# Performance work log

Hardware: AMD Instinct MI355X
Metric: run time of the kernel (lower is better)

The kernel has to match this reference:

```python
import jax, jax.numpy as jnp
import numpy as np

NUM_EXPERTS = 64
TOP_K = 8
HIDDEN = 2048
MLP = 768
TOKENS = 1024


def setup_inputs() -> dict:
    key = jax.random.key(0)
    ks = jax.random.split(key, 5)
    hidden_states = jax.random.normal(ks[0], (TOKENS, HIDDEN), dtype=jnp.float32)
    # lecun-normal-ish scaling (std = 1/sqrt(fan_in))
    router_w = jax.random.normal(ks[1], (HIDDEN, NUM_EXPERTS), dtype=jnp.float32) / np.sqrt(HIDDEN)
    gate_proj = jax.random.normal(ks[2], (NUM_EXPERTS, HIDDEN, MLP), dtype=jnp.float32) / np.sqrt(HIDDEN)
    up_proj = jax.random.normal(ks[3], (NUM_EXPERTS, HIDDEN, MLP), dtype=jnp.float32) / np.sqrt(HIDDEN)
    down_proj = jax.random.normal(ks[4], (NUM_EXPERTS, MLP, HIDDEN), dtype=jnp.float32) / np.sqrt(MLP)
    return {
        "hidden_states": hidden_states,
        "router_w": router_w,
        "gate_proj": gate_proj,
        "up_proj": up_proj,
        "down_proj": down_proj,
    }


def reference(hidden_states, router_w, gate_proj, up_proj, down_proj):
    # Router: [T, E]
    router_logits = hidden_states @ router_w
    # Top-k routing, softmax renormalized over the selected k (norm_topk_prob=True)
    routing_weights, selected_experts = jax.lax.top_k(router_logits, k=TOP_K)
    routing_weights = jax.nn.softmax(routing_weights, axis=-1)  # [T, k]

    sel_flat = selected_experts.ravel()  # [T*k] int32
    # Duplicate each token for each of its k experts: [T*k, H]
    x_exp = jnp.repeat(hidden_states, TOP_K, axis=0)

    # prepare_routing: sort token copies by expert id, count per-expert group sizes
    sort_idx = jnp.argsort(sel_flat)          # stable sort of expert ids
    x_sorted = x_exp[sort_idx]                # [T*k, H] grouped by expert
    group_sizes = jnp.zeros((NUM_EXPERTS,), dtype=jnp.int32).at[sel_flat].add(1)
    unsort_idx = jnp.argsort(sort_idx)

    # Grouped GEMMs (megablox-style) via ragged_dot
    gate_out = jax.lax.ragged_dot(x_sorted, gate_proj, group_sizes)   # [T*k, M]
    up_out = jax.lax.ragged_dot(x_sorted, up_proj, group_sizes)       # [T*k, M]
    down_out = jax.lax.ragged_dot(jax.nn.silu(gate_out) * up_out, down_proj, group_sizes)  # [T*k, H]

    # Unsort back to (token, k) order and combine with routing weights
    unsorted = down_out[unsort_idx].reshape(-1, TOP_K, HIDDEN)
    return jnp.sum(unsorted * routing_weights[..., None], axis=1)  # [T, H]
```

## Files before the change

kernel.cpp:

```cpp
#include <hip/hip_runtime.h>
#include <hip/hip_bf16.h>

#define T_TOKENS 1024
#define HID      2048
#define NEXP     64
#define TOPK     8
#define MLP      768
#define NPAIR    (T_TOKENS * TOPK)

typedef __bf16 bf16x8 __attribute__((ext_vector_type(8)));
typedef float  f32x4  __attribute__((ext_vector_type(4)));
typedef unsigned int u32x2 __attribute__((ext_vector_type(2)));
typedef unsigned int u32x4 __attribute__((ext_vector_type(4)));

#define LDK 40

static __device__ __forceinline__ unsigned short f2bf(float f) {
    __hip_bfloat16 h = __float2bfloat16(f);
    unsigned short u;
    __builtin_memcpy(&u, &h, sizeof(u));
    return u;
}
static __device__ __forceinline__ unsigned int pk2bf(float a, float b) {
    return (unsigned int)f2bf(a) | ((unsigned int)f2bf(b) << 16);
}

__global__ __launch_bounds__(256) void cvt_hs_kernel(
    const float* __restrict__ hs, unsigned short* __restrict__ xb)
{
    int i = (blockIdx.x * 256 + threadIdx.x) * 8;
    f32x4 a = *(const f32x4*)(hs + i);
    f32x4 b = *(const f32x4*)(hs + i + 4);
    u32x4 v;
    v[0] = pk2bf(a[0], a[1]); v[1] = pk2bf(a[2], a[3]);
    v[2] = pk2bf(b[0], b[1]); v[3] = pk2bf(b[2], b[3]);
    *(u32x4*)(xb + i) = v;
}

__global__ __launch_bounds__(256) void router_topk_kernel(
    const float* __restrict__ hs, const float* __restrict__ rw,
    int* __restrict__ sel, float* __restrict__ wts)
{
    const int lane = threadIdx.x & 63;
    const int tg   = threadIdx.x >> 6;
    const int t    = blockIdx.x * 4 + tg;

    const float4* x4 = (const float4*)(hs + (size_t)t * HID);
    float acc = 0.f;
    for (int h4 = 0; h4 < HID / 4; ++h4) {
        float4 xv = x4[h4];
        int hb = h4 * 4 * NEXP + lane;
        acc += xv.x * rw[hb] + xv.y * rw[hb + NEXP]
             + xv.z * rw[hb + 2 * NEXP] + xv.w * rw[hb + 3 * NEXP];
    }

    float v = acc;
    float tv[TOPK]; int ti[TOPK];
    for (int i = 0; i < TOPK; ++i) {
        float m = v; int mi = lane;
        for (int off = 32; off > 0; off >>= 1) {
            float om  = __shfl_xor(m, off, 64);
            int   omi = __shfl_xor(mi, off, 64);
            if (om > m || (om == m && omi < mi)) { m = om; mi = omi; }
        }
        tv[i] = m; ti[i] = mi;
        if (lane == mi) v = -__builtin_inff();
    }
    if (lane == 0) {
        float mx = tv[0], s = 0.f, e[TOPK];
        for (int i = 0; i < TOPK; ++i) { e[i] = __expf(tv[i] - mx); s += e[i]; }
        float inv = 1.f / s;
        for (int i = 0; i < TOPK; ++i) {
            wts[t * TOPK + i] = e[i] * inv;
            sel[t * TOPK + i] = ti[i];
        }
    }
}

__global__ void count_kernel(const int* __restrict__ sel, int* __restrict__ counts)
{
    int p = blockIdx.x * 256 + threadIdx.x;
    if (p < NPAIR) atomicAdd(&counts[sel[p]], 1);
}

__global__ void scan_kernel(const int* __restrict__ counts,
                            int* __restrict__ offsets, int* __restrict__ cursor)
{
    if (threadIdx.x == 0) {
        int s = 0;
        for (int e = 0; e < NEXP; ++e) { offsets[e] = s; cursor[e] = s; s += counts[e]; }
        offsets[NEXP] = s;
    }
}

__global__ void scatter_kernel(const int* __restrict__ sel,
                               int* __restrict__ cursor, int* __restrict__ rows)
{
    int p = blockIdx.x * 256 + threadIdx.x;
    if (p < NPAIR) {
        int e = sel[p];
        int pos = atomicAdd(&cursor[e], 1);
        rows[pos] = p;
    }
}

__global__ __launch_bounds__(512) void gateup_kernel(
    const unsigned short* __restrict__ xb, const float* __restrict__ gw,
    const float* __restrict__ uw, const int* __restrict__ offsets,
    const int* __restrict__ rows, unsigned short* __restrict__ hb)
{
    const int bid = blockIdx.x;
    const int sw  = (bid & 7) * 96 + (bid >> 3);
    const int e   = sw / 12;
    const int n0  = (sw % 12) * 64;

    const int r0 = offsets[e];
    const int nrows = offsets[e + 1] - r0;
    if (nrows <= 0) return;

    __shared__ __align__(16) float smemf[12800];
    unsigned short* smem = (unsigned short*)smemf;

    const int thr  = threadIdx.x;
    const int wave = thr >> 6;
    const int lane = thr & 63;
    const int wg   = wave & 3;
    const int isUp = wave >> 2;
    const int fr   = lane & 15;
    const int fq   = lane >> 4;

    const int ar = thr >> 3;
    const int ac = (thr & 7) * 4;

    const int wk2 = thr & 15;
    const int wnq = (thr & 255) >> 4;
    const float* wsrc = (thr >= 256 ? uw : gw)
        + (size_t)e * HID * MLP + (size_t)(2 * wk2) * MLP + n0 + wnq * 4;
    const int mofs = (thr >= 256) ? 10240 : 7680;

    const int NS = HID / 32;

    for (int m0 = 0; m0 < nrows; m0 += 192) {
        const unsigned short *ap0, *ap1, *ap2;
        bool av0, av1, av2;
        {
            int gr0 = m0 + ar, gr1 = m0 + ar + 64, gr2 = m0 + ar + 128;
            av0 = gr0 < nrows; av1 = gr1 < nrows; av2 = gr2 < nrows;
            int p0 = av0 ? rows[r0 + gr0] : 0;
            int p1 = av1 ? rows[r0 + gr1] : 0;
            int p2 = av2 ? rows[r0 + gr2] : 0;
            ap0 = xb + (size_t)(p0 >> 3) * HID + ac;
            ap1 = xb + (size_t)(p1 >> 3) * HID + ac;
            ap2 = xb + (size_t)(p2 >> 3) * HID + ac;
        }

        u32x2 va0, va1, va2;
        f32x4 w0e, w1e, w0o, w1o;
        const u32x2 z2 = (u32x2){0u, 0u};
        const f32x4 fz = (f32x4){0.f, 0.f, 0.f, 0.f};

        auto LOAD_A = [&](int s) {
            va0 = av0 ? *(const u32x2*)(ap0 + s * 32) : z2;
            va1 = av1 ? *(const u32x2*)(ap1 + s * 32) : z2;
            va2 = av2 ? *(const u32x2*)(ap2 + s * 32) : z2;
        };
        auto WRITE_A = [&](int s) {
            unsigned short* b = smem + (s & 1) * 12800;
            *(u32x2*)(b + ar * LDK + ac) = va0;
            *(u32x2*)(b + (ar + 64) * LDK + ac) = va1;
            *(u32x2*)(b + (ar + 128) * LDK + ac) = va2;
        };
        auto LOAD_WE = [&](int s) {
            const float* wp = wsrc + (size_t)s * 32 * MLP;
            w0e = *(const f32x4*)wp;  w1e = *(const f32x4*)(wp + MLP);
        };
        auto LOAD_WO = [&](int s) {
            const float* wp = wsrc + (size_t)s * 32 * MLP;
            w0o = *(const f32x4*)wp;  w1o = *(const f32x4*)(wp + MLP);
        };
        auto WRITE_WE = [&](int s) {
            unsigned short* wb = smem + (s & 1) * 12800 + mofs;
            #pragma unroll
            for (int i = 0; i < 4; ++i)
                *(unsigned int*)(wb + (wnq * 4 + i) * LDK + 2 * wk2) = pk2bf(w0e[i], w1e[i]);
        };
        auto WRITE_WO = [&](int s) {
            unsigned short* wb = smem + (s & 1) * 12800 + mofs;
            #pragma unroll
            for (int i = 0; i < 4; ++i)
                *(unsigned int*)(wb + (wnq * 4 + i) * LDK + 2 * wk2) = pk2bf(w0o[i], w1o[i]);
        };

        f32x4 acc[3][4];
        #pragma unroll
        for (int ms = 0; ms < 3; ++ms)
            #pragma unroll
            for (int ns = 0; ns < 4; ++ns) acc[ms][ns] = fz;

        const int rem = nrows - m0 - wg * 48;

        auto DOSTEP = [&](const unsigned short* bb) {
            const unsigned short* wbb = bb + mofs;
            bf16x8 aF0, aF1, aF2, wF[4];
            #pragma unroll
            for (int ns = 0; ns < 4; ++ns)
                wF[ns] = *(const bf16x8*)(wbb + (ns * 16 + fr) * LDK + fq * 8);
            aF0 = *(const bf16x8*)(bb + (wg * 48 + fr) * LDK + fq * 8);
            aF1 = *(const bf16x8*)(bb + (wg * 48 + 16 + fr) * LDK + fq * 8);
            aF2 = *(const bf16x8*)(bb + (wg * 48 + 32 + fr) * LDK + fq * 8);
            return (void)0, (void)aF0, (void)aF1, (void)aF2, (void)wF;
        };
        (void)DOSTEP;

        LOAD_WE(0);
        LOAD_WO(1);
        LOAD_A(0);
        WRITE_WE(0);
        WRITE_A(0);
        LOAD_A(1);
        asm volatile("s_waitcnt lgkmcnt(0)" ::: "memory");
        __builtin_amdgcn_s_barrier();

        #define GU_MFMA(BB)                                                          \
        {                                                                            \
            const unsigned short* wbb = (BB) + mofs;                                 \
            bf16x8 aF0, aF1, aF2, wF0, wF1, wF2, wF3;                                \
            wF0 = *(const bf16x8*)(wbb + (0 * 16 + fr) * LDK + fq * 8);              \
            wF1 = *(const bf16x8*)(wbb + (1 * 16 + fr) * LDK + fq * 8);              \
            wF2 = *(const bf16x8*)(wbb + (2 * 16 + fr) * LDK + fq * 8);              \
            wF3 = *(const bf16x8*)(wbb + (3 * 16 + fr) * LDK + fq * 8);              \
            aF0 = *(const bf16x8*)((BB) + (wg * 48 + fr) * LDK + fq * 8);            \
            aF1 = *(const bf16x8*)((BB) + (wg * 48 + 16 + fr) * LDK + fq * 8);       \
            aF2 = *(const bf16x8*)((BB) + (wg * 48 + 32 + fr) * LDK + fq * 8);       \
            MFMA_BLOCK(aF0, aF1, aF2, wF0, wF1, wF2, wF3)                            \
        }
        #define MFMA_BLOCK(A0, A1, A2, W0, W1, W2, W3)                               \
            if (rem > 0) {                                                           \
                acc[0][0] = __builtin_amdgcn_mfma_f32_16x16x32_bf16(A0, W0, acc[0][0], 0, 0, 0); \
                acc[0][1] = __builtin_amdgcn_mfma_f32_16x16x32_bf16(A0, W1, acc[0][1], 0, 0, 0); \
                acc[0][2] = __builtin_amdgcn_mfma_f32_16x16x32_bf16(A0, W2, acc[0][2], 0, 0, 0); \
                acc[0][3] = __builtin_amdgcn_mfma_f32_16x16x32_bf16(A0, W3, acc[0][3], 0, 0, 0); \
            }                                                                        \
            if (rem > 16) {                                                          \
                acc[1][0] = __builtin_amdgcn_mfma_f32_16x16x32_bf16(A1, W0, acc[1][0], 0, 0, 0); \
                acc[1][1] = __builtin_amdgcn_mfma_f32_16x16x32_bf16(A1, W1, acc[1][1], 0, 0, 0); \
                acc[1][2] = __builtin_amdgcn_mfma_f32_16x16x32_bf16(A1, W2, acc[1][2], 0, 0, 0); \
                acc[1][3] = __builtin_amdgcn_mfma_f32_16x16x32_bf16(A1, W3, acc[1][3], 0, 0, 0); \
            }                                                                        \
            if (rem > 32) {                                                          \
                acc[2][0] = __builtin_amdgcn_mfma_f32_16x16x32_bf16(A2, W0, acc[2][0], 0, 0, 0); \
                acc[2][1] = __builtin_amdgcn_mfma_f32_16x16x32_bf16(A2, W1, acc[2][1], 0, 0, 0); \
                acc[2][2] = __builtin_amdgcn_mfma_f32_16x16x32_bf16(A2, W2, acc[2][2], 0, 0, 0); \
                acc[2][3] = __builtin_amdgcn_mfma_f32_16x16x32_bf16(A2, W3, acc[2][3], 0, 0, 0); \
            }

        for (int s = 0; s < NS; s += 2) {
            {
                if (s + 2 < NS) LOAD_WE(s + 2);
                GU_MFMA(smem)
                WRITE_WO(s + 1);
                WRITE_A(s + 1);
                if (s + 2 < NS) LOAD_A(s + 2);
                asm volatile("s_waitcnt lgkmcnt(0)" ::: "memory");
                __builtin_amdgcn_s_barrier();
            }
            {
                if (s + 3 < NS) LOAD_WO(s + 3);
                GU_MFMA(smem + 12800)
                if (s + 2 < NS) { WRITE_WE(s + 2); WRITE_A(s + 2); }
                if (s + 3 < NS) LOAD_A(s + 3);
                asm volatile("s_waitcnt lgkmcnt(0)" ::: "memory");
                __builtin_amdgcn_s_barrier();
            }
        }
        #undef GU_MFMA
        #undef MFMA_BLOCK

        float* xbf = smemf;
        if (isUp) {
            #pragma unroll
            for (int ms = 0; ms < 3; ++ms)
                #pragma unroll
                for (int i = 0; i < 4; ++i) {
                    int lrow = wg * 48 + ms * 16 + fq * 4 + i;
                    #pragma unroll
                    for (int ns = 0; ns < 4; ++ns)
                        xbf[lrow * 65 + ns * 16 + fr] = acc[ms][ns][i];
                }
        }
        __syncthreads();
        if (!isUp) {
            #pragma unroll
            for (int ms = 0; ms < 3; ++ms)
                #pragma unroll
                for (int i = 0; i < 4; ++i) {
                    int lrow = wg * 48 + ms * 16 + fq * 4 + i;
                    int grow = m0 + lrow;
                    if (grow < nrows) {
                        unsigned short* drow = hb + (size_t)(r0 + grow) * MLP + n0;
                        #pragma unroll
                        for (int ns = 0; ns < 4; ++ns) {
                            float g = acc[ms][ns][i];
                            float u = xbf[lrow * 65 + ns * 16 + fr];
                            float h = g * u / (1.f + __expf(-g));
                            drow[ns * 16 + fr] = f2bf(h);
                        }
                    }
                }
        }
        __syncthreads();
    }
}

__global__ __launch_bounds__(256) void down_kernel(
    const unsigned short* __restrict__ hb, const float* __restrict__ dw,
    const int* __restrict__ offsets, const int* __restrict__ rows,
    const float* __restrict__ wts, float* __restrict__ out)
{
    const int bid = blockIdx.x;
    const int sw  = (bid & 7) * 256 + (bid >> 3);
    const int e   = sw >> 5;
    const int n0  = (sw & 31) * 64;

    const int r0 = offsets[e];
    const int nrows = offsets[e + 1] - r0;
    if (nrows <= 0) return;

    __shared__ __align__(16) float smemf[10240];
    unsigned short* smem = (unsigned short*)smemf;

    const int thr  = threadIdx.x;
    const int wave = thr >> 6;
    const int lane = thr & 63;
    const int fr   = lane & 15;
    const int fq   = lane >> 4;

    const int ar = thr >> 2;
    const int ac = (thr & 3) * 8;

    const int wk2 = thr & 15;
    const int wnq = thr >> 4;
    const float* wsrc = dw + (size_t)e * MLP * HID + (size_t)(2 * wk2) * HID + n0 + wnq * 4;

    const int NS = MLP / 32;

    for (int m0 = 0; m0 < nrows; m0 += 192) {
        const bool av0 = (m0 + ar)       < nrows;
        const bool av1 = (m0 + ar + 64)  < nrows;
        const bool av2 = (m0 + ar + 128) < nrows;
        const unsigned short* hp0 = hb + (size_t)(r0 + m0 + ar) * MLP + ac;
        const unsigned short* hp1 = hp0 + (size_t)64  * MLP;
        const unsigned short* hp2 = hp0 + (size_t)128 * MLP;

        u32x4 ua0, ua1, ua2;
        f32x4 w0e, w1e, w0o, w1o;
        const u32x4 uz = (u32x4){0u, 0u, 0u, 0u};
        const f32x4 fz = (f32x4){0.f, 0.f, 0.f, 0.f};

        auto LOAD_A = [&](int s) {
            ua0 = av0 ? *(const u32x4*)(hp0 + s * 32) : uz;
            ua1 = av1 ? *(const u32x4*)(hp1 + s * 32) : uz;
            ua2 = av2 ? *(const u32x4*)(hp2 + s * 32) : uz;
        };
        auto WRITE_A = [&](int s) {
            unsigned short* b = smem + (s & 1) * 10240;
            *(u32x4*)(b + ar * LDK + ac) = ua0;
            *(u32x4*)(b + (ar + 64) * LDK + ac) = ua1;
            *(u32x4*)(b + (ar + 128) * LDK + ac) = ua2;
        };
        auto LOAD_WE = [&](int s) {
            const float* wp = wsrc + (size_t)s * 32 * HID;
            w0e = *(const f32x4*)wp;  w1e = *(const f32x4*)(wp + HID);
        };
        auto LOAD_WO = [&](int s) {
            const float* wp = wsrc + (size_t)s * 32 * HID;
            w0o = *(const f32x4*)wp;  w1o = *(const f32x4*)(wp + HID);
        };
        auto WRITE_WE = [&](int s) {
            unsigned short* wb = smem + (s & 1) * 10240 + 7680;
            #pragma unroll
            for (int i = 0; i < 4; ++i)
                *(unsigned int*)(wb + (wnq * 4 + i) * LDK + 2 * wk2) = pk2bf(w0e[i], w1e[i]);
        };
        auto WRITE_WO = [&](int s) {
            unsigned short* wb = smem + (s & 1) * 10240 + 7680;
            #pragma unroll
            for (int i = 0; i < 4; ++i)
                *(unsigned int*)(wb + (wnq * 4 + i) * LDK + 2 * wk2) = pk2bf(w0o[i], w1o[i]);
        };

        f32x4 acc[3][4];
        #pragma unroll
        for (int ms = 0; ms < 3; ++ms)
            #pragma unroll
            for (int ns = 0; ns < 4; ++ns) acc[ms][ns] = fz;

        const int rem = nrows - m0 - wave * 48;

        LOAD_WE(0);
        LOAD_WO(1);
        LOAD_A(0);
        WRITE_WE(0);
        WRITE_A(0);
        LOAD_A(1);
        asm volatile("s_waitcnt lgkmcnt(0)" ::: "memory");
        __builtin_amdgcn_s_barrier();

        #define DN_MFMA(BB)                                                          \
        {                                                                            \
            const unsigned short* wbb = (BB) + 7680;                                 \
            bf16x8 aF0, aF1, aF2, wF0, wF1, wF2, wF3;                                \
            wF0 = *(const bf16x8*)(wbb + (0 * 16 + fr) * LDK + fq * 8);              \
            wF1 = *(const bf16x8*)(wbb + (1 * 16 + fr) * LDK + fq * 8);              \
            wF2 = *(const bf16x8*)(wbb + (2 * 16 + fr) * LDK + fq * 8);              \
            wF3 = *(const bf16x8*)(wbb + (3 * 16 + fr) * LDK + fq * 8);              \
            aF0 = *(const bf16x8*)((BB) + (wave * 48 + fr) * LDK + fq * 8);          \
            aF1 = *(const bf16x8*)((BB) + (wave * 48 + 16 + fr) * LDK + fq * 8);     \
            aF2 = *(const bf16x8*)((BB) + (wave * 48 + 32 + fr) * LDK + fq * 8);     \
            if (rem > 0) {                                                           \
                acc[0][0] = __builtin_amdgcn_mfma_f32_16x16x32_bf16(aF0, wF0, acc[0][0], 0, 0, 0); \
                acc[0][1] = __builtin_amdgcn_mfma_f32_16x16x32_bf16(aF0, wF1, acc[0][1], 0, 0, 0); \
                acc[0][2] = __builtin_amdgcn_mfma_f32_16x16x32_bf16(aF0, wF2, acc[0][2], 0, 0, 0); \
                acc[0][3] = __builtin_amdgcn_mfma_f32_16x16x32_bf16(aF0, wF3, acc[0][3], 0, 0, 0); \
            }                                                                        \
            if (rem > 16) {                                                          \
                acc[1][0] = __builtin_amdgcn_mfma_f32_16x16x32_bf16(aF1, wF0, acc[1][0], 0, 0, 0); \
                acc[1][1] = __builtin_amdgcn_mfma_f32_16x16x32_bf16(aF1, wF1, acc[1][1], 0, 0, 0); \
                acc[1][2] = __builtin_amdgcn_mfma_f32_16x16x32_bf16(aF1, wF2, acc[1][2], 0, 0, 0); \
                acc[1][3] = __builtin_amdgcn_mfma_f32_16x16x32_bf16(aF1, wF3, acc[1][3], 0, 0, 0); \
            }                                                                        \
            if (rem > 32) {                                                          \
                acc[2][0] = __builtin_amdgcn_mfma_f32_16x16x32_bf16(aF2, wF0, acc[2][0], 0, 0, 0); \
                acc[2][1] = __builtin_amdgcn_mfma_f32_16x16x32_bf16(aF2, wF1, acc[2][1], 0, 0, 0); \
                acc[2][2] = __builtin_amdgcn_mfma_f32_16x16x32_bf16(aF2, wF2, acc[2][2], 0, 0, 0); \
                acc[2][3] = __builtin_amdgcn_mfma_f32_16x16x32_bf16(aF2, wF3, acc[2][3], 0, 0, 0); \
            }                                                                        \
        }

        for (int s = 0; s < NS; s += 2) {
            {
                if (s + 2 < NS) LOAD_WE(s + 2);
                DN_MFMA(smem)
                WRITE_WO(s + 1);
                WRITE_A(s + 1);
                if (s + 2 < NS) LOAD_A(s + 2);
                asm volatile("s_waitcnt lgkmcnt(0)" ::: "memory");
                __builtin_amdgcn_s_barrier();
            }
            {
                if (s + 3 < NS) LOAD_WO(s + 3);
                DN_MFMA(smem + 10240)
                if (s + 2 < NS) { WRITE_WE(s + 2); WRITE_A(s + 2); }
                if (s + 3 < NS) LOAD_A(s + 3);
                asm volatile("s_waitcnt lgkmcnt(0)" ::: "memory");
                __builtin_amdgcn_s_barrier();
            }
        }
        #undef DN_MFMA

        #pragma unroll
        for (int ms = 0; ms < 3; ++ms) {
            #pragma unroll
            for (int i = 0; i < 4; ++i) {
                int lrow = wave * 48 + ms * 16 + fq * 4 + i;
                int grow = m0 + lrow;
                if (grow < nrows) {
                    int p  = rows[r0 + grow];
                    float w = wts[p];
                    float* orow = out + (size_t)(p >> 3) * HID + n0;
                    #pragma unroll
                    for (int ns = 0; ns < 4; ++ns)
                        atomicAdd(orow + ns * 16 + fr, acc[ms][ns][i] * w);
                }
            }
        }
    }
}

extern "C" void kernel_launch(void* const* d_in, const int* in_sizes, int n_in,
                              void* d_out, int out_size, void* d_ws, size_t ws_size,
                              hipStream_t stream)
{
    const float* hs = (const float*)d_in[0];
    const float* rw = (const float*)d_in[1];
    const float* gw = (const float*)d_in[2];
    const float* uw = (const float*)d_in[3];
    const float* dw = (const float*)d_in[4];
    float* out = (float*)d_out;

    char* ws = (char*)d_ws;
    int*   sel     = (int*)(ws);
    float* wts     = (float*)(ws + 32768);
    int*   counts  = (int*)(ws + 65536);
    int*   offsets = (int*)(ws + 65792);
    int*   cursor  = (int*)(ws + 66304);
    int*   rows    = (int*)(ws + 66560);
    unsigned short* xb = (unsigned short*)(ws + 99328);
    unsigned short* hb = (unsigned short*)(ws + 99328 + 4194304);

    hipMemsetAsync(out, 0, (size_t)T_TOKENS * HID * sizeof(float), stream);
    hipMemsetAsync(counts, 0, NEXP * sizeof(int), stream);

    cvt_hs_kernel<<<T_TOKENS * HID / (256 * 8), 256, 0, stream>>>(hs, xb);
    router_topk_kernel<<<T_TOKENS / 4, 256, 0, stream>>>(hs, rw, sel, wts);
    count_kernel<<<NPAIR / 256, 256, 0, stream>>>(sel, counts);
    scan_kernel<<<1, 64, 0, stream>>>(counts, offsets, cursor);
    scatter_kernel<<<NPAIR / 256, 256, 0, stream>>>(sel, cursor, rows);
    gateup_kernel<<<768, 512, 0, stream>>>(xb, gw, uw, offsets, rows, hb);
    down_kernel<<<2048, 256, 0, stream>>>(hb, dw, offsets, rows, wts, out);
}
```

Baseline: 1.237 ms.

## Fuse routing prep kernels, widen per-wave tiles and halve GEMM block counts

Folds the fp32-to-bf16 conversion of hidden states into the router kernel, and merges the count, scan and scatter steps into one single-block kernel that uses shared-memory atomics. The gate/up kernel moves from 512 to 256 threads, with each wave covering 96 rows instead of 48. The down kernel now covers a 128-wide N tile with 2x2 wave tiling, which halves the grid. Weight loads are widened to 8 floats per thread. The aim is to cut launch overhead and raise MFMA work per LDS fragment load, at the cost of more accumulator registers and possible occupancy loss.

```diff
diff --git a/kernel.cpp b/kernel.cpp
--- a/kernel.cpp
+++ b/kernel.cpp
@@ -25,25 +25,28 @@
     return (unsigned int)f2bf(a) | ((unsigned int)f2bf(b) << 16);
 }
 
-__global__ __launch_bounds__(256) void cvt_hs_kernel(
-    const float* __restrict__ hs, unsigned short* __restrict__ xb)
-{
-    int i = (blockIdx.x * 256 + threadIdx.x) * 8;
-    f32x4 a = *(const f32x4*)(hs + i);
-    f32x4 b = *(const f32x4*)(hs + i + 4);
-    u32x4 v;
-    v[0] = pk2bf(a[0], a[1]); v[1] = pk2bf(a[2], a[3]);
-    v[2] = pk2bf(b[0], b[1]); v[3] = pk2bf(b[2], b[3]);
-    *(u32x4*)(xb + i) = v;
-}
-
 __global__ __launch_bounds__(256) void router_topk_kernel(
     const float* __restrict__ hs, const float* __restrict__ rw,
-    int* __restrict__ sel, float* __restrict__ wts)
+    int* __restrict__ sel, float* __restrict__ wts, unsigned short* __restrict__ xb)
 {
     const int lane = threadIdx.x & 63;
     const int tg   = threadIdx.x >> 6;
     const int t    = blockIdx.x * 4 + tg;
+
+    {
+        const float* xr = hs + (size_t)t * HID;
+        unsigned short* xw = xb + (size_t)t * HID;
+        #pragma unroll
+        for (int c = 0; c < 4; ++c) {
+            int i = (lane + c * 64) * 8;
+            f32x4 a = *(const f32x4*)(xr + i);
+            f32x4 b = *(const f32x4*)(xr + i + 4);
+            u32x4 v;
+            v[0] = pk2bf(a[0], a[1]); v[1] = pk2bf(a[2], a[3]);
+            v[2] = pk2bf(b[0], b[1]); v[3] = pk2bf(b[2], b[3]);
+            *(u32x4*)(xw + i) = v;
+        }
+    }
 
     const float4* x4 = (const float4*)(hs + (size_t)t * HID);
     float acc = 0.f;
@@ -77,34 +80,36 @@
     }
 }
 
-__global__ void count_kernel(const int* __restrict__ sel, int* __restrict__ counts)
+__global__ __launch_bounds__(1024) void route_kernel(
+    const int* __restrict__ sel, int* __restrict__ offsets, int* __restrict__ rows)
 {
-    int p = blockIdx.x * 256 + threadIdx.x;
-    if (p < NPAIR) atomicAdd(&counts[sel[p]], 1);
-}
-
-__global__ void scan_kernel(const int* __restrict__ counts,
-                            int* __restrict__ offsets, int* __restrict__ cursor)
-{
-    if (threadIdx.x == 0) {
+    __shared__ int cnt[NEXP];
+    __shared__ int cur[NEXP];
+    const int t = threadIdx.x;
+    if (t < NEXP) cnt[t] = 0;
+    __syncthreads();
+    int e[8];
+    const int p0 = t * 8;
+    #pragma unroll
+    for (int j = 0; j < 8; ++j) {
+        e[j] = sel[p0 + j];
+        atomicAdd(&cnt[e[j]], 1);
+    }
+    __syncthreads();
+    if (t == 0) {
         int s = 0;
-        for (int e = 0; e < NEXP; ++e) { offsets[e] = s; cursor[e] = s; s += counts[e]; }
+        for (int i = 0; i < NEXP; ++i) { cur[i] = s; offsets[i] = s; s += cnt[i]; }
         offsets[NEXP] = s;
     }
-}
-
-__global__ void scatter_kernel(const int* __restrict__ sel,
-                               int* __restrict__ cursor, int* __restrict__ rows)
-{
-    int p = blockIdx.x * 256 + threadIdx.x;
-    if (p < NPAIR) {
-        int e = sel[p];
-        int pos = atomicAdd(&cursor[e], 1);
-        rows[pos] = p;
-    }
-}
-
-__global__ __launch_bounds__(512) void gateup_kernel(
+    __syncthreads();
+    #pragma unroll
+    for (int j = 0; j < 8; ++j) {
+        int pos = atomicAdd(&cur[e[j]], 1);
+        rows[pos] = p0 + j;
+    }
+}
+
+__global__ __launch_bounds__(256, 2) void gateup_kernel(
     const unsigned short* __restrict__ xb, const float* __restrict__ gw,
     const float* __restrict__ uw, const int* __restrict__ offsets,
     const int* __restrict__ rows, unsigned short* __restrict__ hb)
@@ -124,19 +129,21 @@
     const int thr  = threadIdx.x;
     const int wave = thr >> 6;
     const int lane = thr & 63;
-    const int wg   = wave & 3;
-    const int isUp = wave >> 2;
+    const int wg   = wave & 1;
+    const int isUp = wave >> 1;
     const int fr   = lane & 15;
     const int fq   = lane >> 4;
-
-    const int ar = thr >> 3;
-    const int ac = (thr & 7) * 4;
-
-    const int wk2 = thr & 15;
-    const int wnq = (thr & 255) >> 4;
-    const float* wsrc = (thr >= 256 ? uw : gw)
-        + (size_t)e * HID * MLP + (size_t)(2 * wk2) * MLP + n0 + wnq * 4;
-    const int mofs = (thr >= 256) ? 10240 : 7680;
+    const int mofs_c = isUp ? 10240 : 7680;
+
+    const int ar = thr >> 2;
+    const int ac = (thr & 3) * 8;
+
+    const int tt   = thr & 127;
+    const int wk2  = tt & 15;
+    const int nst  = (tt >> 4) * 8;
+    const float* wsrc = (thr >= 128 ? uw : gw)
+        + (size_t)e * HID * MLP + (size_t)(2 * wk2) * MLP + n0 + nst;
+    const int mofs_s = (thr >= 128) ? 10240 : 7680;
 
     const int NS = HID / 32;
 
@@ -154,63 +161,77 @@
             ap2 = xb + (size_t)(p2 >> 3) * HID + ac;
         }
 
-        u32x2 va0, va1, va2;
-        f32x4 w0e, w1e, w0o, w1o;
-        const u32x2 z2 = (u32x2){0u, 0u};
+        u32x4 va0, va1, va2;
+        f32x4 wAe, wBe, wCe, wDe, wAo, wBo, wCo, wDo;
+        const u32x4 uz = (u32x4){0u, 0u, 0u, 0u};
         const f32x4 fz = (f32x4){0.f, 0.f, 0.f, 0.f};
 
         auto LOAD_A = [&](int s) {
-            va0 = av0 ? *(const u32x2*)(ap0 + s * 32) : z2;
-            va1 = av1 ? *(const u32x2*)(ap1 + s * 32) : z2;
-            va2 = av2 ? *(const u32x2*)(ap2 + s * 32) : z2;
+            va0 = av0 ? *(const u32x4*)(ap0 + s * 32) : uz;
+            va1 = av1 ? *(const u32x4*)(ap1 + s * 32) : uz;
+            va2 = av2 ? *(const u32x4*)(ap2 + s * 32) : uz;
         };
         auto WRITE_A = [&](int s) {
             unsigned short* b = smem + (s & 1) * 12800;
-            *(u32x2*)(b + ar * LDK + ac) = va0;
-            *(u32x2*)(b + (ar + 64) * LDK + ac) = va1;
-            *(u32x2*)(b + (ar + 128) * LDK + ac) = va2;
+            *(u32x4*)(b + ar * LDK + ac) = va0;
+            *(u32x4*)(b + (ar + 64) * LDK + ac) = va1;
+            *(u32x4*)(b + (ar + 128) * LDK + ac) = va2;
         };
         auto LOAD_WE = [&](int s) {
             const float* wp = wsrc + (size_t)s * 32 * MLP;
-            w0e = *(const f32x4*)wp;  w1e = *(const f32x4*)(wp + MLP);
+            wAe = *(const f32x4*)wp;        wBe = *(const f32x4*)(wp + 4);
+            wCe = *(const f32x4*)(wp + MLP); wDe = *(const f32x4*)(wp + MLP + 4);
         };
         auto LOAD_WO = [&](int s) {
             const float* wp = wsrc + (size_t)s * 32 * MLP;
-            w0o = *(const f32x4*)wp;  w1o = *(const f32x4*)(wp + MLP);
+            wAo = *(const f32x4*)wp;        wBo = *(const f32x4*)(wp + 4);
+            wCo = *(const f32x4*)(wp + MLP); wDo = *(const f32x4*)(wp + MLP + 4);
         };
         auto WRITE_WE = [&](int s) {
-            unsigned short* wb = smem + (s & 1) * 12800 + mofs;
-            #pragma unroll
-            for (int i = 0; i < 4; ++i)
-                *(unsigned int*)(wb + (wnq * 4 + i) * LDK + 2 * wk2) = pk2bf(w0e[i], w1e[i]);
+            unsigned short* wb = smem + (s & 1) * 12800 + mofs_s;
+            #pragma unroll
+            for (int j = 0; j < 4; ++j) {
+                *(unsigned int*)(wb + (nst + j) * LDK + 2 * wk2)     = pk2bf(wAe[j], wCe[j]);
+                *(unsigned int*)(wb + (nst + 4 + j) * LDK + 2 * wk2) = pk2bf(wBe[j], wDe[j]);
+            }
         };
         auto WRITE_WO = [&](int s) {
-            unsigned short* wb = smem + (s & 1) * 12800 + mofs;
-            #pragma unroll
-            for (int i = 0; i < 4; ++i)
-                *(unsigned int*)(wb + (wnq * 4 + i) * LDK + 2 * wk2) = pk2bf(w0o[i], w1o[i]);
-        };
-
-        f32x4 acc[3][4];
+            unsigned short* wb = smem + (s & 1) * 12800 + mofs_s;
+            #pragma unroll
+            for (int j = 0; j < 4; ++j) {
+                *(unsigned int*)(wb + (nst + j) * LDK + 2 * wk2)     = pk2bf(wAo[j], wCo[j]);
+                *(unsigned int*)(wb + (nst + 4 + j) * LDK + 2 * wk2) = pk2bf(wBo[j], wDo[j]);
+            }
+        };
+
+        f32x4 acc[6][4];
         #pragma unroll
-        for (int ms = 0; ms < 3; ++ms)
+        for (int ms = 0; ms < 6; ++ms)
             #pragma unroll
             for (int ns = 0; ns < 4; ++ns) acc[ms][ns] = fz;
 
-        const int rem = nrows - m0 - wg * 48;
-
-        auto DOSTEP = [&](const unsigned short* bb) {
-            const unsigned short* wbb = bb + mofs;
-            bf16x8 aF0, aF1, aF2, wF[4];
-            #pragma unroll
-            for (int ns = 0; ns < 4; ++ns)
-                wF[ns] = *(const bf16x8*)(wbb + (ns * 16 + fr) * LDK + fq * 8);
-            aF0 = *(const bf16x8*)(bb + (wg * 48 + fr) * LDK + fq * 8);
-            aF1 = *(const bf16x8*)(bb + (wg * 48 + 16 + fr) * LDK + fq * 8);
-            aF2 = *(const bf16x8*)(bb + (wg * 48 + 32 + fr) * LDK + fq * 8);
-            return (void)0, (void)aF0, (void)aF1, (void)aF2, (void)wF;
-        };
-        (void)DOSTEP;
+        const int rem = nrows - m0 - wg * 96;
+
+        auto STEP = [&](const unsigned short* bb) {
+            const unsigned short* wbb = bb + mofs_c;
+            bf16x8 wF0 = *(const bf16x8*)(wbb + (0 * 16 + fr) * LDK + fq * 8);
+            bf16x8 wF1 = *(const bf16x8*)(wbb + (1 * 16 + fr) * LDK + fq * 8);
+            bf16x8 wF2 = *(const bf16x8*)(wbb + (2 * 16 + fr) * LDK + fq * 8);
+            bf16x8 wF3 = *(const bf16x8*)(wbb + (3 * 16 + fr) * LDK + fq * 8);
+            bf16x8 aF[6];
+            #pragma unroll
+            for (int ms = 0; ms < 6; ++ms)
+                aF[ms] = *(const bf16x8*)(bb + (wg * 96 + ms * 16 + fr) * LDK + fq * 8);
+            #pragma unroll
+            for (int ms = 0; ms < 6; ++ms) {
+                if (rem > ms * 16) {
+                    acc[ms][0] = __builtin_amdgcn_mfma_f32_16x16x32_bf16(aF[ms], wF0, acc[ms][0], 0, 0, 0);
+                    acc[ms][1] = __builtin_amdgcn_mfma_f32_16x16x32_bf16(aF[ms], wF1, acc[ms][1], 0, 0, 0);
+                    acc[ms][2] = __builtin_amdgcn_mfma_f32_16x16x32_bf16(aF[ms], wF2, acc[ms][2], 0, 0, 0);
+                    acc[ms][3] = __builtin_amdgcn_mfma_f32_16x16x32_bf16(aF[ms], wF3, acc[ms][3], 0, 0, 0);
+                }
+            }
+        };
 
         LOAD_WE(0);
         LOAD_WO(1);
@@ -221,68 +242,29 @@
         asm volatile("s_waitcnt lgkmcnt(0)" ::: "memory");
         __builtin_amdgcn_s_barrier();
 
-        #define GU_MFMA(BB)                                                          \
-        {                                                                            \
-            const unsigned short* wbb = (BB) + mofs;                                 \
-            bf16x8 aF0, aF1, aF2, wF0, wF1, wF2, wF3;                                \
-            wF0 = *(const bf16x8*)(wbb + (0 * 16 + fr) * LDK + fq * 8);              \
-            wF1 = *(const bf16x8*)(wbb + (1 * 16 + fr) * LDK + fq * 8);              \
-            wF2 = *(const bf16x8*)(wbb + (2 * 16 + fr) * LDK + fq * 8);              \
-            wF3 = *(const bf16x8*)(wbb + (3 * 16 + fr) * LDK + fq * 8);              \
-            aF0 = *(const bf16x8*)((BB) + (wg * 48 + fr) * LDK + fq * 8);            \
-            aF1 = *(const bf16x8*)((BB) + (wg * 48 + 16 + fr) * LDK + fq * 8);       \
-            aF2 = *(const bf16x8*)((BB) + (wg * 48 + 32 + fr) * LDK + fq * 8);       \
-            MFMA_BLOCK(aF0, aF1, aF2, wF0, wF1, wF2, wF3)                            \
-        }
-        #define MFMA_BLOCK(A0, A1, A2, W0, W1, W2, W3)                               \
-            if (rem > 0) {                                                           \
-                acc[0][0] = __builtin_amdgcn_mfma_f32_16x16x32_bf16(A0, W0, acc[0][0], 0, 0, 0); \
-                acc[0][1] = __builtin_amdgcn_mfma_f32_16x16x32_bf16(A0, W1, acc[0][1], 0, 0, 0); \
-                acc[0][2] = __builtin_amdgcn_mfma_f32_16x16x32_bf16(A0, W2, acc[0][2], 0, 0, 0); \
-                acc[0][3] = __builtin_amdgcn_mfma_f32_16x16x32_bf16(A0, W3, acc[0][3], 0, 0, 0); \
-            }                                                                        \
-            if (rem > 16) {                                                          \
-                acc[1][0] = __builtin_amdgcn_mfma_f32_16x16x32_bf16(A1, W0, acc[1][0], 0, 0, 0); \
-                acc[1][1] = __builtin_amdgcn_mfma_f32_16x16x32_bf16(A1, W1, acc[1][1], 0, 0, 0); \
-                acc[1][2] = __builtin_amdgcn_mfma_f32_16x16x32_bf16(A1, W2, acc[1][2], 0, 0, 0); \
-                acc[1][3] = __builtin_amdgcn_mfma_f32_16x16x32_bf16(A1, W3, acc[1][3], 0, 0, 0); \
-            }                                                                        \
-            if (rem > 32) {                                                          \
-                acc[2][0] = __builtin_amdgcn_mfma_f32_16x16x32_bf16(A2, W0, acc[2][0], 0, 0, 0); \
-                acc[2][1] = __builtin_amdgcn_mfma_f32_16x16x32_bf16(A2, W1, acc[2][1], 0, 0, 0); \
-                acc[2][2] = __builtin_amdgcn_mfma_f32_16x16x32_bf16(A2, W2, acc[2][2], 0, 0, 0); \
-                acc[2][3] = __builtin_amdgcn_mfma_f32_16x16x32_bf16(A2, W3, acc[2][3], 0, 0, 0); \
-            }
-
         for (int s = 0; s < NS; s += 2) {
-            {
-                if (s + 2 < NS) LOAD_WE(s + 2);
-                GU_MFMA(smem)
-                WRITE_WO(s + 1);
-                WRITE_A(s + 1);
-                if (s + 2 < NS) LOAD_A(s + 2);
-                asm volatile("s_waitcnt lgkmcnt(0)" ::: "memory");
-                __builtin_amdgcn_s_barrier();
-            }
-            {
-                if (s + 3 < NS) LOAD_WO(s + 3);
-                GU_MFMA(smem + 12800)
-                if (s + 2 < NS) { WRITE_WE(s + 2); WRITE_A(s + 2); }
-                if (s + 3 < NS) LOAD_A(s + 3);
-                asm volatile("s_waitcnt lgkmcnt(0)" ::: "memory");
-                __builtin_amdgcn_s_barrier();
-            }
-        }
-        #undef GU_MFMA
-        #undef MFMA_BLOCK
+            if (s + 2 < NS) LOAD_WE(s + 2);
+            STEP(smem);
+            WRITE_WO(s + 1);
+            WRITE_A(s + 1);
+            if (s + 2 < NS) LOAD_A(s + 2);
+            asm volatile("s_waitcnt lgkmcnt(0)" ::: "memory");
+            __builtin_amdgcn_s_barrier();
+            if (s + 3 < NS) LOAD_WO(s + 3);
+            STEP(smem + 12800);
+            if (s + 2 < NS) { WRITE_WE(s + 2); WRITE_A(s + 2); }
+            if (s + 3 < NS) LOAD_A(s + 3);
+            asm volatile("s_waitcnt lgkmcnt(0)" ::: "memory");
+            __builtin_amdgcn_s_barrier();
+        }
 
         float* xbf = smemf;
         if (isUp) {
             #pragma unroll
-            for (int ms = 0; ms < 3; ++ms)
+            for (int ms = 0; ms < 6; ++ms)
                 #pragma unroll
                 for (int i = 0; i < 4; ++i) {
-                    int lrow = wg * 48 + ms * 16 + fq * 4 + i;
+                    int lrow = wg * 96 + ms * 16 + fq * 4 + i;
                     #pragma unroll
                     for (int ns = 0; ns < 4; ++ns)
                         xbf[lrow * 65 + ns * 16 + fr] = acc[ms][ns][i];
@@ -291,10 +273,10 @@
         __syncthreads();
         if (!isUp) {
             #pragma unroll
-            for (int ms = 0; ms < 3; ++ms)
+            for (int ms = 0; ms < 6; ++ms)
                 #pragma unroll
                 for (int i = 0; i < 4; ++i) {
-                    int lrow = wg * 48 + ms * 16 + fq * 4 + i;
+                    int lrow = wg * 96 + ms * 16 + fq * 4 + i;
                     int grow = m0 + lrow;
                     if (grow < nrows) {
                         unsigned short* drow = hb + (size_t)(r0 + grow) * MLP + n0;
@@ -312,26 +294,28 @@
     }
 }
 
-__global__ __launch_bounds__(256) void down_kernel(
+__global__ __launch_bounds__(256, 2) void down_kernel(
     const unsigned short* __restrict__ hb, const float* __restrict__ dw,
     const int* __restrict__ offsets, const int* __restrict__ rows,
     const float* __restrict__ wts, float* __restrict__ out)
 {
     const int bid = blockIdx.x;
-    const int sw  = (bid & 7) * 256 + (bid >> 3);
-    const int e   = sw >> 5;
-    const int n0  = (sw & 31) * 64;
+    const int sw  = (bid & 7) * 128 + (bid >> 3);
+    const int e   = sw >> 4;
+    const int n0  = (sw & 15) * 128;
 
     const int r0 = offsets[e];
     const int nrows = offsets[e + 1] - r0;
     if (nrows <= 0) return;
 
-    __shared__ __align__(16) float smemf[10240];
+    __shared__ __align__(16) float smemf[12800];
     unsigned short* smem = (unsigned short*)smemf;
 
     const int thr  = threadIdx.x;
     const int wave = thr >> 6;
     const int lane = thr & 63;
+    const int wg   = wave & 1;
+    const int wn   = wave >> 1;
     const int fr   = lane & 15;
     const int fq   = lane >> 4;
 
@@ -339,8 +323,8 @@
     const int ac = (thr & 3) * 8;
 
     const int wk2 = thr & 15;
-    const int wnq = thr >> 4;
-    const float* wsrc = dw + (size_t)e * MLP * HID + (size_t)(2 * wk2) * HID + n0 + wnq * 4;
+    const int nst = (thr >> 4) * 8;
+    const float* wsrc = dw + (size_t)e * MLP * HID + (size_t)(2 * wk2) * HID + n0 + nst;
 
     const int NS = MLP / 32;
 
@@ -353,7 +337,7 @@
         const unsigned short* hp2 = hp0 + (size_t)128 * MLP;
 
         u32x4 ua0, ua1, ua2;
-        f32x4 w0e, w1e, w0o, w1o;
+        f32x4 wAe, wBe, wCe, wDe, wAo, wBo, wCo, wDo;
         const u32x4 uz = (u32x4){0u, 0u, 0u, 0u};
         const f32x4 fz = (f32x4){0.f, 0.f, 0.f, 0.f};
 
@@ -363,39 +347,66 @@
             ua2 = av2 ? *(const u32x4*)(hp2 + s * 32) : uz;
         };
         auto WRITE_A = [&](int s) {
-            unsigned short* b = smem + (s & 1) * 10240;
+            unsigned short* b = smem + (s & 1) * 12800;
             *(u32x4*)(b + ar * LDK + ac) = ua0;
             *(u32x4*)(b + (ar + 64) * LDK + ac) = ua1;
             *(u32x4*)(b + (ar + 128) * LDK + ac) = ua2;
         };
         auto LOAD_WE = [&](int s) {
             const float* wp = wsrc + (size_t)s * 32 * HID;
-            w0e = *(const f32x4*)wp;  w1e = *(const f32x4*)(wp + HID);
+            wAe = *(const f32x4*)wp;        wBe = *(const f32x4*)(wp + 4);
+            wCe = *(const f32x4*)(wp + HID); wDe = *(const f32x4*)(wp + HID + 4);
         };
         auto LOAD_WO = [&](int s) {
             const float* wp = wsrc + (size_t)s * 32 * HID;
-            w0o = *(const f32x4*)wp;  w1o = *(const f32x4*)(wp + HID);
+            wAo = *(const f32x4*)wp;        wBo = *(const f32x4*)(wp + 4);
+            wCo = *(const f32x4*)(wp + HID); wDo = *(const f32x4*)(wp + HID + 4);
         };
         auto WRITE_WE = [&](int s) {
-            unsigned short* wb = smem + (s & 1) * 10240 + 7680;
-            #pragma unroll
-            for (int i = 0; i < 4; ++i)
-                *(unsigned int*)(wb + (wnq * 4 + i) * LDK + 2 * wk2) = pk2bf(w0e[i], w1e[i]);
+            unsigned short* wb = smem + (s & 1) * 12800 + 7680;
+            #pragma unroll
+            for (int j = 0; j < 4; ++j) {
+                *(unsigned int*)(wb + (nst + j) * LDK + 2 * wk2)     = pk2bf(wAe[j], wCe[j]);
+                *(unsigned int*)(wb + (nst + 4 + j) * LDK + 2 * wk2) = pk2bf(wBe[j], wDe[j]);
+            }
         };
         auto WRITE_WO = [&](int s) {
-            unsigned short* wb = smem + (s & 1) * 10240 + 7680;
-            #pragma unroll
-            for (int i = 0; i < 4; ++i)
-                *(unsigned int*)(wb + (wnq * 4 + i) * LDK + 2 * wk2) = pk2bf(w0o[i], w1o[i]);
-        };
-
-        f32x4 acc[3][4];
+            unsigned short* wb = smem + (s & 1) * 12800 + 7680;
+            #pragma unroll
+            for (int j = 0; j < 4; ++j) {
+                *(unsigned int*)(wb + (nst + j) * LDK + 2 * wk2)     = pk2bf(wAo[j], wCo[j]);
+                *(unsigned int*)(wb + (nst + 4 + j) * LDK + 2 * wk2) = pk2bf(wBo[j], wDo[j]);
+            }
+        };
+
+        f32x4 acc[6][4];
         #pragma unroll
-        for (int ms = 0; ms < 3; ++ms)
+        for (int ms = 0; ms < 6; ++ms)
             #pragma unroll
             for (int ns = 0; ns < 4; ++ns) acc[ms][ns] = fz;
 
-        const int rem = nrows - m0 - wave * 48;
+        const int rem = nrows - m0 - wg * 96;
+
+        auto STEP = [&](const unsigned short* bb) {
+            const unsigned short* wbb = bb + 7680;
+            bf16x8 wF0 = *(const bf16x8*)(wbb + (wn * 64 + 0 * 16 + fr) * LDK + fq * 8);
+            bf16x8 wF1 = *(const bf16x8*)(wbb + (wn * 64 + 1 * 16 + fr) * LDK + fq * 8);
+            bf16x8 wF2 = *(const bf16x8*)(wbb + (wn * 64 + 2 * 16 + fr) * LDK + fq * 8);
+            bf16x8 wF3 = *(const bf16x8*)(wbb + (wn * 64 + 3 * 16 + fr) * LDK + fq * 8);
+            bf16x8 aF[6];
+            #pragma unroll
+            for (int ms = 0; ms < 6; ++ms)
+                aF[ms] = *(const bf16x8*)(bb + (wg * 96 + ms * 16 + fr) * LDK + fq * 8);
+            #pragma unroll
+            for (int ms = 0; ms < 6; ++ms) {
+                if (rem > ms * 16) {
+                    acc[ms][0] = __builtin_amdgcn_mfma_f32_16x16x32_bf16(aF[ms], wF0, acc[ms][0], 0, 0, 0);
+                    acc[ms][1] = __builtin_amdgcn_mfma_f32_16x16x32_bf16(aF[ms], wF1, acc[ms][1], 0, 0, 0);
+                    acc[ms][2] = __builtin_amdgcn_mfma_f32_16x16x32_bf16(aF[ms], wF2, acc[ms][2], 0, 0, 0);
+                    acc[ms][3] = __builtin_amdgcn_mfma_f32_16x16x32_bf16(aF[ms], wF3, acc[ms][3], 0, 0, 0);
+                }
+            }
+        };
 
         LOAD_WE(0);
         LOAD_WO(1);
@@ -406,74 +417,39 @@
         asm volatile("s_waitcnt lgkmcnt(0)" ::: "memory");
         __builtin_amdgcn_s_barrier();
 
-        #define DN_MFMA(BB)                                                          \
-        {                                                                            \
-            const unsigned short* wbb = (BB) + 7680;                                 \
-            bf16x8 aF0, aF1, aF2, wF0, wF1, wF2, wF3;                                \
-            wF0 = *(const bf16x8*)(wbb + (0 * 16 + fr) * LDK + fq * 8);              \
-            wF1 = *(const bf16x8*)(wbb + (1 * 16 + fr) * LDK + fq * 8);              \
-            wF2 = *(const bf16x8*)(wbb + (2 * 16 + fr) * LDK + fq * 8);              \
-            wF3 = *(const bf16x8*)(wbb + (3 * 16 + fr) * LDK + fq * 8);              \
-            aF0 = *(const bf16x8*)((BB) + (wave * 48 + fr) * LDK + fq * 8);          \
-            aF1 = *(const bf16x8*)((BB) + (wave * 48 + 16 + fr) * LDK + fq * 8);     \
-            aF2 = *(const bf16x8*)((BB) + (wave * 48 + 32 + fr) * LDK + fq * 8);     \
-            if (rem > 0) {                                                           \
-                acc[0][0] = __builtin_amdgcn_mfma_f32_16x16x32_bf16(aF0, wF0, acc[0][0], 0, 0, 0); \
-                acc[0][1] = __builtin_amdgcn_mfma_f32_16x16x32_bf16(aF0, wF1, acc[0][1], 0, 0, 0); \
-                acc[0][2] = __builtin_amdgcn_mfma_f32_16x16x32_bf16(aF0, wF2, acc[0][2], 0, 0, 0); \
-                acc[0][3] = __builtin_amdgcn_mfma_f32_16x16x32_bf16(aF0, wF3, acc[0][3], 0, 0, 0); \
-            }                                                                        \
-            if (rem > 16) {                                                          \
-                acc[1][0] = __builtin_amdgcn_mfma_f32_16x16x32_bf16(aF1, wF0, acc[1][0], 0, 0, 0); \
-                acc[1][1] = __builtin_amdgcn_mfma_f32_16x16x32_bf16(aF1, wF1, acc[1][1], 0, 0, 0); \
-                acc[1][2] = __builtin_amdgcn_mfma_f32_16x16x32_bf16(aF1, wF2, acc[1][2], 0, 0, 0); \
-                acc[1][3] = __builtin_amdgcn_mfma_f32_16x16x32_bf16(aF1, wF3, acc[1][3], 0, 0, 0); \
-            }                                                                        \
-            if (rem > 32) {                                                          \
-                acc[2][0] = __builtin_amdgcn_mfma_f32_16x16x32_bf16(aF2, wF0, acc[2][0], 0, 0, 0); \
-                acc[2][1] = __builtin_amdgcn_mfma_f32_16x16x32_bf16(aF2, wF1, acc[2][1], 0, 0, 0); \
-                acc[2][2] = __builtin_amdgcn_mfma_f32_16x16x32_bf16(aF2, wF2, acc[2][2], 0, 0, 0); \
-                acc[2][3] = __builtin_amdgcn_mfma_f32_16x16x32_bf16(aF2, wF3, acc[2][3], 0, 0, 0); \
-            }                                                                        \
-        }
-
         for (int s = 0; s < NS; s += 2) {
-            {
-                if (s + 2 < NS) LOAD_WE(s + 2);
-                DN_MFMA(smem)
-                WRITE_WO(s + 1);
-                WRITE_A(s + 1);
-                if (s + 2 < NS) LOAD_A(s + 2);
-                asm volatile("s_waitcnt lgkmcnt(0)" ::: "memory");
-                __builtin_amdgcn_s_barrier();
-            }
-            {
-                if (s + 3 < NS) LOAD_WO(s + 3);
-                DN_MFMA(smem + 10240)
-                if (s + 2 < NS) { WRITE_WE(s + 2); WRITE_A(s + 2); }
-                if (s + 3 < NS) LOAD_A(s + 3);
-                asm volatile("s_waitcnt lgkmcnt(0)" ::: "memory");
-                __builtin_amdgcn_s_barrier();
-            }
-        }
-        #undef DN_MFMA
+            if (s + 2 < NS) LOAD_WE(s + 2);
+            STEP(smem);
+            WRITE_WO(s + 1);
+            WRITE_A(s + 1);
+            if (s + 2 < NS) LOAD_A(s + 2);
+            asm volatile("s_waitcnt lgkmcnt(0)" ::: "memory");
+            __builtin_amdgcn_s_barrier();
+            if (s + 3 < NS) LOAD_WO(s + 3);
+            STEP(smem + 12800);
+            if (s + 2 < NS) { WRITE_WE(s + 2); WRITE_A(s + 2); }
+            if (s + 3 < NS) LOAD_A(s + 3);
+            asm volatile("s_waitcnt lgkmcnt(0)" ::: "memory");
+            __builtin_amdgcn_s_barrier();
+        }
 
         #pragma unroll
-        for (int ms = 0; ms < 3; ++ms) {
+        for (int ms = 0; ms < 6; ++ms) {
             #pragma unroll
             for (int i = 0; i < 4; ++i) {
-                int lrow = wave * 48 + ms * 16 + fq * 4 + i;
+                int lrow = wg * 96 + ms * 16 + fq * 4 + i;
                 int grow = m0 + lrow;
                 if (grow < nrows) {
                     int p  = rows[r0 + grow];
                     float w = wts[p];
-                    float* orow = out + (size_t)(p >> 3) * HID + n0;
+                    float* orow = out + (size_t)(p >> 3) * HID + n0 + wn * 64;
                     #pragma unroll
                     for (int ns = 0; ns < 4; ++ns)
                         atomicAdd(orow + ns * 16 + fr, acc[ms][ns][i] * w);
                 }
             }
         }
+        __syncthreads();
     }
 }
 
@@ -491,21 +467,15 @@
     char* ws = (char*)d_ws;
     int*   sel     = (int*)(ws);
     float* wts     = (float*)(ws + 32768);
-    int*   counts  = (int*)(ws + 65536);
     int*   offsets = (int*)(ws + 65792);
-    int*   cursor  = (int*)(ws + 66304);
     int*   rows    = (int*)(ws + 66560);
     unsigned short* xb = (unsigned short*)(ws + 99328);
     unsigned short* hb = (unsigned short*)(ws + 99328 + 4194304);
 
     hipMemsetAsync(out, 0, (size_t)T_TOKENS * HID * sizeof(float), stream);
-    hipMemsetAsync(counts, 0, NEXP * sizeof(int), stream);
-
-    cvt_hs_kernel<<<T_TOKENS * HID / (256 * 8), 256, 0, stream>>>(hs, xb);
-    router_topk_kernel<<<T_TOKENS / 4, 256, 0, stream>>>(hs, rw, sel, wts);
-    count_kernel<<<NPAIR / 256, 256, 0, stream>>>(sel, counts);
-    scan_kernel<<<1, 64, 0, stream>>>(counts, offsets, cursor);
-    scatter_kernel<<<NPAIR / 256, 256, 0, stream>>>(sel, cursor, rows);
-    gateup_kernel<<<768, 512, 0, stream>>>(xb, gw, uw, offsets, rows, hb);
-    down_kernel<<<2048, 256, 0, stream>>>(hb, dw, offsets, rows, wts, out);
-}
+
+    router_topk_kernel<<<T_TOKENS / 4, 256, 0, stream>>>(hs, rw, sel, wts, xb);
+    route_kernel<<<1, 1024, 0, stream>>>(sel, offsets, rows);
+    gateup_kernel<<<768, 256, 0, stream>>>(xb, gw, uw, offsets, rows, hb);
+    down_kernel<<<1024, 256, 0, stream>>>(hb, dw, offsets, rows, wts, out);
+}
```

New measurement: 1.198 ms. -3.2%, faster.
